# Kernel optimization log

Measured on AMD Instinct MI355X. Metric: run time of the kernel, lower is better.

## Reference

```python
import jax, jax.numpy as jnp
import numpy as np

SEQ, B, IN, H, L = 256, 512, 300, 512, 256
EPS = 1e-5


def setup_inputs() -> dict:
    key = jax.random.key(0)
    ks = jax.random.split(key, 10)
    s_ih = 1.0 / np.sqrt(H)
    return {
        "x": jax.random.normal(ks[0], (SEQ, B, IN), dtype=jnp.float32),
        "W_ih": jax.random.normal(ks[1], (4 * H, IN), dtype=jnp.float32) * s_ih,
        "W_hh": jax.random.normal(ks[2], (4 * H, H), dtype=jnp.float32) * s_ih,
        "b_ih": jax.random.normal(ks[3], (4 * H,), dtype=jnp.float32) * s_ih,
        "b_hh": jax.random.normal(ks[4], (4 * H,), dtype=jnp.float32) * s_ih,
        "bn1_gamma": jnp.ones((H,), dtype=jnp.float32),
        "bn1_beta": jnp.zeros((H,), dtype=jnp.float32),
        "W1": jax.random.normal(ks[5], (L, H), dtype=jnp.float32) / np.sqrt(H),
        "b1": jax.random.normal(ks[6], (L,), dtype=jnp.float32) * 0.01,
        "bn2_gamma": jnp.ones((L,), dtype=jnp.float32),
        "bn2_beta": jnp.zeros((L,), dtype=jnp.float32),
        "W2": jax.random.normal(ks[7], (1, L), dtype=jnp.float32) / np.sqrt(L),
        "b2": jax.random.normal(ks[8], (1,), dtype=jnp.float32) * 0.01,
    }


def _batchnorm(x, gamma, beta):
    # training-mode BatchNorm1d: batch statistics, biased variance
    mean = jnp.mean(x, axis=0)
    var = jnp.var(x, axis=0)
    return (x - mean) * jax.lax.rsqrt(var + EPS) * gamma + beta


def reference(x, W_ih, W_hh, b_ih, b_hh, bn1_gamma, bn1_beta, W1, b1,
              bn2_gamma, bn2_beta, W2, b2):
    # Pre-compute the input projection for all timesteps in one big GEMM:
    # [S, B, IN] @ [IN, 4H] -> [S, B, 4H]
    x_proj = jnp.einsum('sbi,gi->sbg', x, W_ih) + b_ih + b_hh

    def step(carry, xt):
        h, c = carry
        gates = xt + h @ W_hh.T  # [B, 4H]
        i, f, g, o = jnp.split(gates, 4, axis=-1)
        i = jax.nn.sigmoid(i)
        f = jax.nn.sigmoid(f)
        g = jnp.tanh(g)
        o = jax.nn.sigmoid(o)
        c = f * c + i * g
        h = o * jnp.tanh(c)
        return (h, c), None

    h0 = jnp.zeros((x.shape[1], H), dtype=x.dtype)
    c0 = jnp.zeros((x.shape[1], H), dtype=x.dtype)
    (h, _c), _ = jax.lax.scan(step, (h0, c0), x_proj)
    # dropout with training=False -> identity

    h = _batchnorm(h, bn1_gamma, bn1_beta)
    h = h @ W1.T + b1
    h = _batchnorm(h, bn2_gamma, bn2_beta)
    h = jax.nn.relu(h)
    out = h @ W2.T + b2            # [B, 1]
    out = 4.0 * jax.nn.sigmoid(out)
    return out.squeeze(-1)         # [B]
```

## Files before the change

### kernel.cpp

```cpp
#include <hip/hip_runtime.h>
#include <math.h>

constexpr int SEQ   = 256;
constexpr int BATCH = 512;
constexpr int INDIM = 300;
constexpr int KIH   = 320;
constexpr int HDIM  = 512;
constexpr int LDIM  = 256;
constexpr int G4    = 4 * HDIM;

typedef _Float16 f16x8 __attribute__((ext_vector_type(8)));
typedef _Float16 f16x4 __attribute__((ext_vector_type(4)));
typedef float    f32x4 __attribute__((ext_vector_type(4)));


__global__ __launch_bounds__(256) void prep_weights_kernel(
    const float* __restrict__ Wih, const float* __restrict__ Whh,
    const float* __restrict__ bih, const float* __restrict__ bhh,
    _Float16* __restrict__ slab, float* __restrict__ bsum)
{
    const int by = blockIdx.x >> 6;
    const int rl = blockIdx.x & 63;
    const int g  = rl >> 4, r = rl & 15;
    const int grow = g * HDIM + by * 16 + r;
    const int tid = threadIdx.x;
    if (tid < 208) {
        const int col0 = tid * 4;
        f16x4 v;
        #pragma unroll
        for (int e = 0; e < 4; ++e) {
            const int col = col0 + e;
            float f;
            if (col < KIH) f = (col < INDIM) ? Wih[(size_t)grow * INDIM + col] : 0.f;
            else           f = Whh[(size_t)grow * HDIM + (col - KIH)];
            v[e] = (_Float16)f;
        }
        *(f16x4*)(slab + ((size_t)(by * 64 + rl)) * 832 + col0) = v;
    } else if (tid == 208) {
        bsum[grow] = bih[grow] + bhh[grow];
    }
}

__global__ __launch_bounds__(256) void prep_x_kernel(
    const float* __restrict__ x, _Float16* __restrict__ xall)
{
    const int rowl = threadIdx.x >> 6;
    const int s    = threadIdx.x & 63;
    const int row  = blockIdx.x * 4 + rowl;
    if (s >= 40) return;
    const int k0 = s * 8;
    const float* xr = x + (size_t)row * INDIM;
    f16x8 v;
    #pragma unroll
    for (int e = 0; e < 8; ++e)
        v[e] = (k0 + e < INDIM) ? (_Float16)xr[k0 + e] : (_Float16)0.f;
    *(f16x8*)(xall + (size_t)row * KIH + k0) = v;
}

__global__ __launch_bounds__(512, 2) void lstm_persist10(
    const _Float16* __restrict__ xall,
    const _Float16* __restrict__ slab,
    _Float16* __restrict__ hb,
    float* __restrict__ h32,
    const float* __restrict__ bsum,
    int* __restrict__ cnt)
{
    __shared__ _Float16 act[13][64][64];
    __shared__ float    Gb2[2][64][68];

    const int tid  = threadIdx.x;
    const int wid  = tid >> 6;
    const int lane = tid & 63;
    const int gg   = wid >> 2;
    const int bh   = (wid >> 1) & 1;
    const int ks   = wid & 1;
    const int l15  = lane & 15;
    const int q4   = lane >> 4;
    const int bx   = blockIdx.x & 7;
    const int by   = blockIdx.x >> 3;
    const int b0   = bx * 64;
    const int hc0  = by * 16;

    f16x8 ws[13][2];
    {
        const _Float16* sb = slab + (size_t)by * 64 * 832
                                  + (size_t)(gg * 32 + l15) * 832 + ks * 32 + q4 * 8;
        #pragma unroll
        for (int ch = 0; ch < 13; ++ch)
            #pragma unroll
            for (int mt = 0; mt < 2; ++mt) {
                const unsigned long long* p = (const unsigned long long*)
                    (sb + (size_t)mt * 16 * 832 + ch * 64);
                union { unsigned long long u[2]; f16x8 v; } w;
                w.u[0] = __hip_atomic_load(p,     __ATOMIC_RELAXED,
                                           __HIP_MEMORY_SCOPE_AGENT);
                w.u[1] = __hip_atomic_load(p + 1, __ATOMIC_RELAXED,
                                           __HIP_MEMORY_SCOPE_AGENT);
                ws[ch][mt] = w.v;
            }
    }

    const int srow  = tid >> 3;
    const int suu   = tid & 7;
    const int wbyte = srow * 128 + ((suu ^ (srow & 7)) << 4);

    int rbyte[2];
    #pragma unroll
    for (int bt = 0; bt < 2; ++bt) {
        const int row  = bh * 32 + bt * 16 + l15;
        const int unit = ks * 4 + q4;
        rbyte[bt] = row * 128 + ((unit ^ (row & 7)) << 4);
    }

    const int bl  = tid >> 3;
    const int j0l = (tid & 7) * 2;
    const int bg  = b0 + bl;
    const int jg  = hc0 + j0l;
    float bsv[4][2];
    #pragma unroll
    for (int g = 0; g < 4; ++g) {
        bsv[g][0] = bsum[g * HDIM + jg];
        bsv[g][1] = bsum[g * HDIM + jg + 1];
    }
    float cv0 = 0.f, cv1 = 0.f;

#define BARX() do { asm volatile("" ::: "memory");                           \
                    __builtin_amdgcn_s_barrier();                            \
                    asm volatile("" ::: "memory"); } while (0)
#define LGKM0() asm volatile("s_waitcnt lgkmcnt(0)" ::: "memory")
#define VM0()   asm volatile("s_waitcnt vmcnt(0)" ::: "memory")

    const _Float16* xpt = xall + (size_t)(b0 + srow) * KIH + suu * 8;
    const _Float16* hpt = hb + (size_t)(b0 + srow) * HDIM + suu * 8;

    f16x8 xcur[5], xnxt[5];
    #pragma unroll
    for (int ch = 0; ch < 5; ++ch)
        xcur[ch] = *(const f16x8*)(xpt + ch * 64);

    for (int t = 0; t < SEQ; ++t) {
        #pragma unroll
        for (int ch = 0; ch < 5; ++ch)
            *(f16x8*)((char*)&act[ch][0][0] + wbyte) = xcur[ch];

        if (t > 0) {
            const int* fp = cnt + bx * 32 + (lane & 31);
            int wd = 0;
            for (;;) {
                const int f = __hip_atomic_load(fp, __ATOMIC_RELAXED,
                                                __HIP_MEMORY_SCOPE_AGENT);
                if (__all(f >= t)) break;
                if (++wd > (1 << 20)) break;
                __builtin_amdgcn_s_sleep(1);
            }
            asm volatile("" ::: "memory");
        }

        {
            const _Float16* hbase = hpt + (size_t)(t & 1) * BATCH * HDIM;
            f16x8 hr[8];
            #pragma unroll
            for (int j = 0; j < 8; ++j) {
                const unsigned long long* p = (const unsigned long long*)
                    (hbase + j * 64);
                union { unsigned long long u[2]; f16x8 v; } hv;
                hv.u[0] = __hip_atomic_load(p,     __ATOMIC_RELAXED,
                                            __HIP_MEMORY_SCOPE_AGENT);
                hv.u[1] = __hip_atomic_load(p + 1, __ATOMIC_RELAXED,
                                            __HIP_MEMORY_SCOPE_AGENT);
                hr[j] = hv.v;
            }
            #pragma unroll
            for (int j = 0; j < 8; ++j)
                *(f16x8*)((char*)&act[5 + j][0][0] + wbyte) = hr[j];
        }
        LGKM0(); BARX();

        {
            const _Float16* xnb = xpt + (size_t)(t + 1) * BATCH * KIH;
            #pragma unroll
            for (int ch = 0; ch < 5; ++ch)
                xnxt[ch] = *(const f16x8*)(xnb + ch * 64);
        }

        f32x4 acc00 = {0.f,0.f,0.f,0.f}, acc01 = {0.f,0.f,0.f,0.f};
        f32x4 acc10 = {0.f,0.f,0.f,0.f}, acc11 = {0.f,0.f,0.f,0.f};
        #pragma unroll
        for (int ch = 0; ch < 13; ++ch) {
            const char* base = (const char*)&act[ch][0][0];
            const f16x8 bf0 = *(const f16x8*)(base + rbyte[0]);
            const f16x8 bf1 = *(const f16x8*)(base + rbyte[1]);
            acc00 = __builtin_amdgcn_mfma_f32_16x16x32_f16(ws[ch][0], bf0, acc00, 0, 0, 0);
            acc01 = __builtin_amdgcn_mfma_f32_16x16x32_f16(ws[ch][0], bf1, acc01, 0, 0, 0);
            acc10 = __builtin_amdgcn_mfma_f32_16x16x32_f16(ws[ch][1], bf0, acc10, 0, 0, 0);
            acc11 = __builtin_amdgcn_mfma_f32_16x16x32_f16(ws[ch][1], bf1, acc11, 0, 0, 0);
        }

        #pragma unroll
        for (int q = 0; q < 4; ++q) {
            Gb2[ks][gg * 32 +      q4 * 4 + q][bh * 32 +      l15] = acc00[q];
            Gb2[ks][gg * 32 +      q4 * 4 + q][bh * 32 + 16 + l15] = acc01[q];
            Gb2[ks][gg * 32 + 16 + q4 * 4 + q][bh * 32 +      l15] = acc10[q];
            Gb2[ks][gg * 32 + 16 + q4 * 4 + q][bh * 32 + 16 + l15] = acc11[q];
        }
        LGKM0(); BARX();

        {
            float pre[4][2];
            #pragma unroll
            for (int g = 0; g < 4; ++g) {
                pre[g][0] = Gb2[0][g * 16 + j0l    ][bl]
                          + Gb2[1][g * 16 + j0l    ][bl] + bsv[g][0];
                pre[g][1] = Gb2[0][g * 16 + j0l + 1][bl]
                          + Gb2[1][g * 16 + j0l + 1][bl] + bsv[g][1];
            }
            float hv0, hv1;
            {
                float vi = 1.f / (1.f + __expf(-pre[0][0]));
                float vf = 1.f / (1.f + __expf(-pre[1][0]));
                float vg = 1.f - 2.f / (__expf(2.f * pre[2][0]) + 1.f);
                float vo = 1.f / (1.f + __expf(-pre[3][0]));
                const float cc = vf * cv0 + vi * vg;
                cv0 = cc;
                hv0 = vo * (1.f - 2.f / (__expf(2.f * cc) + 1.f));
            }
            {
                float vi = 1.f / (1.f + __expf(-pre[0][1]));
                float vf = 1.f / (1.f + __expf(-pre[1][1]));
                float vg = 1.f - 2.f / (__expf(2.f * pre[2][1]) + 1.f);
                float vo = 1.f / (1.f + __expf(-pre[3][1]));
                const float cc = vf * cv1 + vi * vg;
                cv1 = cc;
                hv1 = vo * (1.f - 2.f / (__expf(2.f * cc) + 1.f));
            }
            union { unsigned int u; _Float16 v[2]; } hu;
            hu.v[0] = (_Float16)hv0; hu.v[1] = (_Float16)hv1;
            _Float16* hbw = hb + (size_t)((t + 1) & 1) * BATCH * HDIM;
            __hip_atomic_store((unsigned int*)(hbw + (size_t)bg * HDIM + jg),
                               hu.u, __ATOMIC_RELAXED, __HIP_MEMORY_SCOPE_AGENT);
            if (t == SEQ - 1) {
                float* hp = h32 + (size_t)bg * HDIM + jg;
                hp[0] = hv0; hp[1] = hv1;
            }
        }
        VM0(); BARX();
        if (tid == 0)
            __hip_atomic_store(&cnt[bx * 32 + by], t + 1, __ATOMIC_RELAXED,
                               __HIP_MEMORY_SCOPE_AGENT);

        #pragma unroll
        for (int ch = 0; ch < 5; ++ch) xcur[ch] = xnxt[ch];
    }
#undef BARX
#undef LGKM0
#undef VM0
}

__global__ __launch_bounds__(256) void prep_kernel(
    const float* __restrict__ Wih, const float* __restrict__ Whh,
    const float* __restrict__ bih, const float* __restrict__ bhh,
    _Float16* __restrict__ Wihc, _Float16* __restrict__ Whhc,
    float* __restrict__ bsum)
{
    const int g = blockIdx.x;
    for (int col = threadIdx.x; col < KIH; col += 256)
        Wihc[(size_t)g * KIH + col] =
            (col < INDIM) ? (_Float16)Wih[(size_t)g * INDIM + col] : (_Float16)0.f;
    for (int col = threadIdx.x; col < HDIM; col += 256)
        Whhc[(size_t)g * HDIM + col] = (_Float16)Whh[(size_t)g * HDIM + col];
    if (threadIdx.x == 0) bsum[g] = bih[g] + bhh[g];
}

__global__ __launch_bounds__(256) void fused_step_kernel(
    const float* __restrict__ xt, const _Float16* __restrict__ Wihc,
    const _Float16* __restrict__ Whhc, const float* __restrict__ bsum,
    float* __restrict__ c, float* __restrict__ h)
{
    __shared__ _Float16 As[32][72];
    __shared__ _Float16 Bs[128][72];
    __shared__ float    Gb[4][32][36];

    const int tid = threadIdx.x;
    const int b0  = blockIdx.x * 32;
    const int hc0 = blockIdx.y * 32;
    const int wid  = tid >> 6;
    const int lane = tid & 63;

    f32x4 acc[2][2] = {};
    const int arow = tid >> 3;
    const int ac8  = (tid & 7) * 8;
    const int brr  = tid >> 1;
    const int bseg = (tid & 1) * 32;

    for (int phase = 0; phase < 2; ++phase) {
        const float* Asrc = phase ? h : xt;
        const _Float16* Bsrc = phase ? Whhc : Wihc;
        const int Kpad = phase ? HDIM : KIH;
        const int Kval = phase ? HDIM : INDIM;
        const int astr = phase ? HDIM : INDIM;

        for (int k0 = 0; k0 < Kpad; k0 += 64) {
            const int gk = k0 + ac8;
            const float* pa = Asrc + (size_t)(b0 + arow) * astr + gk;
            float4 u = {0.f,0.f,0.f,0.f}, v = {0.f,0.f,0.f,0.f};
            if (gk + 3 < Kval)  u = *(const float4*)pa;
            if (gk + 7 < Kval)  v = *(const float4*)(pa + 4);
            f16x8 a8;
            a8[0]=(_Float16)u.x; a8[1]=(_Float16)u.y; a8[2]=(_Float16)u.z; a8[3]=(_Float16)u.w;
            a8[4]=(_Float16)v.x; a8[5]=(_Float16)v.y; a8[6]=(_Float16)v.z; a8[7]=(_Float16)v.w;
            const int grow = (brr >> 5) * HDIM + hc0 + (brr & 31);
            const _Float16* pb = Bsrc + (size_t)grow * Kpad + k0 + bseg;
            f16x8 w0 = *(const f16x8*)(pb + 0);
            f16x8 w1 = *(const f16x8*)(pb + 8);
            f16x8 w2 = *(const f16x8*)(pb + 16);
            f16x8 w3 = *(const f16x8*)(pb + 24);
            __syncthreads();
            *(f16x8*)&As[arow][ac8] = a8;
            *(f16x8*)&Bs[brr][bseg + 0]  = w0;
            *(f16x8*)&Bs[brr][bseg + 8]  = w1;
            *(f16x8*)&Bs[brr][bseg + 16] = w2;
            *(f16x8*)&Bs[brr][bseg + 24] = w3;
            __syncthreads();
            const int lr = lane & 15;
            const int lk = (lane >> 4) * 8;
            #pragma unroll
            for (int kf = 0; kf < 2; ++kf) {
                const int kl = kf * 32 + lk;
                f16x8 a0 = *(const f16x8*)&As[lr][kl];
                f16x8 a1 = *(const f16x8*)&As[16 + lr][kl];
                f16x8 bb0 = *(const f16x8*)&Bs[wid * 32 + lr][kl];
                f16x8 bb1 = *(const f16x8*)&Bs[wid * 32 + 16 + lr][kl];
                acc[0][0] = __builtin_amdgcn_mfma_f32_16x16x32_f16(a0, bb0, acc[0][0], 0, 0, 0);
                acc[0][1] = __builtin_amdgcn_mfma_f32_16x16x32_f16(a0, bb1, acc[0][1], 0, 0, 0);
                acc[1][0] = __builtin_amdgcn_mfma_f32_16x16x32_f16(a1, bb0, acc[1][0], 0, 0, 0);
                acc[1][1] = __builtin_amdgcn_mfma_f32_16x16x32_f16(a1, bb1, acc[1][1], 0, 0, 0);
            }
        }
    }
    __syncthreads();
    {
        const int cn = lane & 15;
        const int rbq = (lane >> 4) * 4;
        #pragma unroll
        for (int mi = 0; mi < 2; ++mi)
            #pragma unroll
            for (int ni = 0; ni < 2; ++ni)
                #pragma unroll
                for (int r = 0; r < 4; ++r)
                    Gb[wid][mi * 16 + rbq + r][ni * 16 + cn] = acc[mi][ni][r];
    }
    __syncthreads();
    {
        const int bl  = tid >> 3;
        const int jl0 = (tid & 7) * 4;
        const int gb  = b0 + bl;
        const int gj  = hc0 + jl0;
        const f32x4 ig = *(const f32x4*)&Gb[0][bl][jl0];
        const f32x4 fg = *(const f32x4*)&Gb[1][bl][jl0];
        const f32x4 gg = *(const f32x4*)&Gb[2][bl][jl0];
        const f32x4 og = *(const f32x4*)&Gb[3][bl][jl0];
        const f32x4 bi = *(const f32x4*)&bsum[0 * HDIM + gj];
        const f32x4 bf = *(const f32x4*)&bsum[1 * HDIM + gj];
        const f32x4 bg = *(const f32x4*)&bsum[2 * HDIM + gj];
        const f32x4 bo = *(const f32x4*)&bsum[3 * HDIM + gj];
        float* cp = c + (size_t)gb * HDIM + gj;
        float* hp = h + (size_t)gb * HDIM + gj;
        f32x4 cvv = *(const f32x4*)cp;
        f32x4 hv;
        #pragma unroll
        for (int q = 0; q < 4; ++q) {
            const float iv = 1.f / (1.f + __expf(-(ig[q] + bi[q])));
            const float fv = 1.f / (1.f + __expf(-(fg[q] + bf[q])));
            const float gv = tanhf(gg[q] + bg[q]);
            const float ov = 1.f / (1.f + __expf(-(og[q] + bo[q])));
            const float cc = fv * cvv[q] + iv * gv;
            cvv[q] = cc;
            hv[q] = ov * tanhf(cc);
        }
        *(f32x4*)cp = cvv;
        *(f32x4*)hp = hv;
    }
}

__global__ __launch_bounds__(256) void bn_stats_kernel(
    const float* __restrict__ X, int nfeat,
    const float* __restrict__ gamma, const float* __restrict__ beta,
    float* __restrict__ s, float* __restrict__ t)
{
    const int f = blockIdx.x * 256 + threadIdx.x;
    if (f >= nfeat) return;
    float sum = 0.f, sq = 0.f;
    for (int b = 0; b < BATCH; ++b) {
        const float v = X[(size_t)b * nfeat + f];
        sum += v; sq += v * v;
    }
    const float mean = sum * (1.f / BATCH);
    const float var  = sq * (1.f / BATCH) - mean * mean;
    const float rstd = rsqrtf(var + 1e-5f);
    const float sc   = gamma[f] * rstd;
    s[f] = sc;
    t[f] = beta[f] - mean * sc;
}

__global__ __launch_bounds__(256) void fc1_kernel(
    const float* __restrict__ h, const float* __restrict__ s1,
    const float* __restrict__ t1, const float* __restrict__ W1,
    const float* __restrict__ b1, float* __restrict__ out1)
{
    const int b = blockIdx.x;
    const int l = threadIdx.x;
    const float* hbp = h  + (size_t)b * HDIM;
    const float* wl  = W1 + (size_t)l * HDIM;
    float acc = 0.f;
    for (int k = 0; k < HDIM; ++k)
        acc += (hbp[k] * s1[k] + t1[k]) * wl[k];
    out1[(size_t)b * LDIM + l] = acc + b1[l];
}

__global__ __launch_bounds__(256) void final_kernel(
    const float* __restrict__ out1, const float* __restrict__ s2,
    const float* __restrict__ t2, const float* __restrict__ W2,
    const float* __restrict__ b2, float* __restrict__ out)
{
    const int b = blockIdx.x;
    float v = out1[(size_t)b * LDIM + threadIdx.x];
    v = v * s2[threadIdx.x] + t2[threadIdx.x];
    v = fmaxf(v, 0.f);
    v *= W2[threadIdx.x];
    #pragma unroll
    for (int off = 32; off > 0; off >>= 1) v += __shfl_down(v, off);
    __shared__ float red[4];
    if ((threadIdx.x & 63) == 0) red[threadIdx.x >> 6] = v;
    __syncthreads();
    if (threadIdx.x == 0) {
        const float ssum = red[0] + red[1] + red[2] + red[3] + b2[0];
        out[b] = 4.f / (1.f + expf(-ssum));
    }
}

extern "C" void kernel_launch(void* const* d_in, const int* in_sizes, int n_in,
                              void* d_out, int out_size, void* d_ws, size_t ws_size,
                              hipStream_t stream) {
    const float* x   = (const float*)d_in[0];
    const float* Wih = (const float*)d_in[1];
    const float* Whh = (const float*)d_in[2];
    const float* bih = (const float*)d_in[3];
    const float* bhh = (const float*)d_in[4];
    const float* g1  = (const float*)d_in[5];
    const float* be1 = (const float*)d_in[6];
    const float* W1  = (const float*)d_in[7];
    const float* b1  = (const float*)d_in[8];
    const float* g2  = (const float*)d_in[9];
    const float* be2 = (const float*)d_in[10];
    const float* W2  = (const float*)d_in[11];
    const float* b2  = (const float*)d_in[12];
    float* out = (float*)d_out;

    const size_t SZ_XALL = (size_t)(SEQ + 1) * BATCH * KIH * 2;
    const size_t SZ_SLAB = (size_t)32 * 64 * 832 * 2;
    const size_t SZ_HB   = (size_t)2 * BATCH * HDIM * 2;
    const size_t SZ_H32  = (size_t)BATCH * HDIM * 4;
    const size_t SZ_BSUM = (size_t)G4 * 4;
    const size_t SZ_CNT  = (size_t)SEQ * 8 * 4;
    const size_t SZ_ST   = (size_t)(HDIM * 2 + LDIM * 2) * 4;
    const size_t SZ_OUT1 = (size_t)BATCH * LDIM * 4;
    const size_t NEED = SZ_XALL + SZ_SLAB + SZ_HB + SZ_H32 + SZ_BSUM +
                        SZ_CNT + SZ_ST + SZ_OUT1;

    if (ws_size >= NEED) {
        char* p = (char*)d_ws;
        _Float16* xall = (_Float16*)p;           p += SZ_XALL;
        _Float16* slab = (_Float16*)p;           p += SZ_SLAB;
        _Float16* hbuf = (_Float16*)p;           p += SZ_HB;
        float* h32     = (float*)p;              p += SZ_H32;
        float* bsum    = (float*)p;              p += SZ_BSUM;
        int*   cnt     = (int*)p;                p += SZ_CNT;
        float* s1 = (float*)p;                   p += HDIM * 4;
        float* t1 = (float*)p;                   p += HDIM * 4;
        float* s2 = (float*)p;                   p += LDIM * 4;
        float* t2 = (float*)p;                   p += LDIM * 4;
        float* out1 = (float*)p;

        hipMemsetAsync(hbuf, 0, SZ_HB, stream);
        hipMemsetAsync(cnt, 0, SZ_CNT, stream);
        prep_weights_kernel<<<2048, 256, 0, stream>>>(Wih, Whh, bih, bhh, slab, bsum);
        prep_x_kernel<<<SEQ * 128, 256, 0, stream>>>(x, xall);

        lstm_persist10<<<dim3(256), dim3(512), 0, stream>>>(
            xall, slab, hbuf, h32, bsum, cnt);

        bn_stats_kernel<<<2, 256, 0, stream>>>(h32, HDIM, g1, be1, s1, t1);
        fc1_kernel<<<BATCH, 256, 0, stream>>>(h32, s1, t1, W1, b1, out1);
        bn_stats_kernel<<<1, 256, 0, stream>>>(out1, LDIM, g2, be2, s2, t2);
        final_kernel<<<BATCH, 256, 0, stream>>>(out1, s2, t2, W2, b2, out);
    } else {
        float* ws   = (float*)d_ws;
        float* h    = ws;
        float* c    = h + BATCH * HDIM;
        float* bsum = c + BATCH * HDIM;
        float* s1   = bsum + G4;
        float* t1   = s1 + HDIM;
        float* s2   = t1 + HDIM;
        float* t2   = s2 + LDIM;
        float* out1 = t2 + LDIM;
        _Float16* Wihc = (_Float16*)(out1 + (size_t)BATCH * LDIM);
        _Float16* Whhc = Wihc + (size_t)G4 * KIH;

        hipMemsetAsync(h, 0, (size_t)2 * BATCH * HDIM * sizeof(float), stream);
        prep_kernel<<<G4, 256, 0, stream>>>(Wih, Whh, bih, bhh, Wihc, Whhc, bsum);
        const dim3 sgrid(BATCH / 32, HDIM / 32);
        for (int t = 0; t < SEQ; ++t) {
            fused_step_kernel<<<sgrid, 256, 0, stream>>>(
                x + (size_t)t * BATCH * INDIM, Wihc, Whhc, bsum, c, h);
        }
        bn_stats_kernel<<<2, 256, 0, stream>>>(h, HDIM, g1, be1, s1, t1);
        fc1_kernel<<<BATCH, 256, 0, stream>>>(h, s1, t1, W1, b1, out1);
        bn_stats_kernel<<<1, 256, 0, stream>>>(out1, LDIM, g2, be2, s2, t2);
        final_kernel<<<BATCH, 256, 0, stream>>>(out1, s2, t2, W2, b2, out);
    }
}
```

Baseline: 1.419 ms.

## Overlap input-projection MFMAs with cross-block flag wait in persistent LSTM

Splits the per-step gate GEMM into the x-projection chunks and the recurrent h chunks. Waves 1-7 compute the five x chunks while wave 0 spins on the inter-block completion counters, and wave 0 does its own x chunks after the barrier. Only the h-dependent chunks then wait for the new hidden state. This hides part of the global synchronisation latency behind independent MFMA work, at the cost of an extra barrier per step and a less even spread of work across waves.

```diff
diff --git a/kernel.cpp b/kernel.cpp
--- a/kernel.cpp
+++ b/kernel.cpp
@@ -57,7 +57,7 @@
     *(f16x8*)(xall + (size_t)row * KIH + k0) = v;
 }
 
-__global__ __launch_bounds__(512, 2) void lstm_persist10(
+__global__ __launch_bounds__(512, 2) void lstm_persist11(
     const _Float16* __restrict__ xall,
     const _Float16* __restrict__ slab,
     _Float16* __restrict__ hb,
@@ -130,6 +130,16 @@
 #define LGKM0() asm volatile("s_waitcnt lgkmcnt(0)" ::: "memory")
 #define VM0()   asm volatile("s_waitcnt vmcnt(0)" ::: "memory")
 
+#define MFMA_CHUNK(CH) do {                                                  \
+        const char* base = (const char*)&act[CH][0][0];                      \
+        const f16x8 bf0 = *(const f16x8*)(base + rbyte[0]);                  \
+        const f16x8 bf1 = *(const f16x8*)(base + rbyte[1]);                  \
+        acc00 = __builtin_amdgcn_mfma_f32_16x16x32_f16(ws[CH][0], bf0, acc00, 0, 0, 0); \
+        acc01 = __builtin_amdgcn_mfma_f32_16x16x32_f16(ws[CH][0], bf1, acc01, 0, 0, 0); \
+        acc10 = __builtin_amdgcn_mfma_f32_16x16x32_f16(ws[CH][1], bf0, acc10, 0, 0, 0); \
+        acc11 = __builtin_amdgcn_mfma_f32_16x16x32_f16(ws[CH][1], bf1, acc11, 0, 0, 0); \
+    } while (0)
+
     const _Float16* xpt = xall + (size_t)(b0 + srow) * KIH + suu * 8;
     const _Float16* hpt = hb + (size_t)(b0 + srow) * HDIM + suu * 8;
 
@@ -142,23 +152,33 @@
         #pragma unroll
         for (int ch = 0; ch < 5; ++ch)
             *(f16x8*)((char*)&act[ch][0][0] + wbyte) = xcur[ch];
-
-        if (t > 0) {
-            const int* fp = cnt + bx * 32 + (lane & 31);
-            int wd = 0;
-            for (;;) {
-                const int f = __hip_atomic_load(fp, __ATOMIC_RELAXED,
-                                                __HIP_MEMORY_SCOPE_AGENT);
-                if (__all(f >= t)) break;
-                if (++wd > (1 << 20)) break;
-                __builtin_amdgcn_s_sleep(1);
-            }
-            asm volatile("" ::: "memory");
-        }
-
+        LGKM0(); BARX();
+
+        f32x4 acc00 = {0.f,0.f,0.f,0.f}, acc01 = {0.f,0.f,0.f,0.f};
+        f32x4 acc10 = {0.f,0.f,0.f,0.f}, acc11 = {0.f,0.f,0.f,0.f};
+
+        if (wid == 0) {
+            if (t > 0) {
+                const int* fp = cnt + bx * 32 + (lane & 31);
+                int wd = 0;
+                for (;;) {
+                    const int f = __hip_atomic_load(fp, __ATOMIC_RELAXED,
+                                                    __HIP_MEMORY_SCOPE_AGENT);
+                    if (__all(f >= t)) break;
+                    if (++wd > (1 << 20)) break;
+                    __builtin_amdgcn_s_sleep(2);
+                }
+                asm volatile("" ::: "memory");
+            }
+        } else {
+            MFMA_CHUNK(0); MFMA_CHUNK(1); MFMA_CHUNK(2);
+            MFMA_CHUNK(3); MFMA_CHUNK(4);
+        }
+        BARX();
+
+        f16x8 hr[8];
         {
             const _Float16* hbase = hpt + (size_t)(t & 1) * BATCH * HDIM;
-            f16x8 hr[8];
             #pragma unroll
             for (int j = 0; j < 8; ++j) {
                 const unsigned long long* p = (const unsigned long long*)
@@ -170,31 +190,24 @@
                                             __HIP_MEMORY_SCOPE_AGENT);
                 hr[j] = hv.v;
             }
-            #pragma unroll
-            for (int j = 0; j < 8; ++j)
-                *(f16x8*)((char*)&act[5 + j][0][0] + wbyte) = hr[j];
-        }
-        LGKM0(); BARX();
-
+        }
+        if (wid == 0) {
+            MFMA_CHUNK(0); MFMA_CHUNK(1); MFMA_CHUNK(2);
+            MFMA_CHUNK(3); MFMA_CHUNK(4);
+        }
         {
             const _Float16* xnb = xpt + (size_t)(t + 1) * BATCH * KIH;
             #pragma unroll
             for (int ch = 0; ch < 5; ++ch)
                 xnxt[ch] = *(const f16x8*)(xnb + ch * 64);
         }
-
-        f32x4 acc00 = {0.f,0.f,0.f,0.f}, acc01 = {0.f,0.f,0.f,0.f};
-        f32x4 acc10 = {0.f,0.f,0.f,0.f}, acc11 = {0.f,0.f,0.f,0.f};
-        #pragma unroll
-        for (int ch = 0; ch < 13; ++ch) {
-            const char* base = (const char*)&act[ch][0][0];
-            const f16x8 bf0 = *(const f16x8*)(base + rbyte[0]);
-            const f16x8 bf1 = *(const f16x8*)(base + rbyte[1]);
-            acc00 = __builtin_amdgcn_mfma_f32_16x16x32_f16(ws[ch][0], bf0, acc00, 0, 0, 0);
-            acc01 = __builtin_amdgcn_mfma_f32_16x16x32_f16(ws[ch][0], bf1, acc01, 0, 0, 0);
-            acc10 = __builtin_amdgcn_mfma_f32_16x16x32_f16(ws[ch][1], bf0, acc10, 0, 0, 0);
-            acc11 = __builtin_amdgcn_mfma_f32_16x16x32_f16(ws[ch][1], bf1, acc11, 0, 0, 0);
-        }
+        #pragma unroll
+        for (int j = 0; j < 8; ++j)
+            *(f16x8*)((char*)&act[5 + j][0][0] + wbyte) = hr[j];
+        LGKM0(); BARX();
+
+        MFMA_CHUNK(5); MFMA_CHUNK(6); MFMA_CHUNK(7); MFMA_CHUNK(8);
+        MFMA_CHUNK(9); MFMA_CHUNK(10); MFMA_CHUNK(11); MFMA_CHUNK(12);
 
         #pragma unroll
         for (int q = 0; q < 4; ++q) {
@@ -254,6 +267,7 @@
 #undef BARX
 #undef LGKM0
 #undef VM0
+#undef MFMA_CHUNK
 }
 
 __global__ __launch_bounds__(256) void prep_kernel(
@@ -486,7 +500,7 @@
         prep_weights_kernel<<<2048, 256, 0, stream>>>(Wih, Whh, bih, bhh, slab, bsum);
         prep_x_kernel<<<SEQ * 128, 256, 0, stream>>>(x, xall);
 
-        lstm_persist10<<<dim3(256), dim3(512), 0, stream>>>(
+        lstm_persist11<<<dim3(256), dim3(512), 0, stream>>>(
             xall, slab, hbuf, h32, bsum, cnt);
 
         bn_stats_kernel<<<2, 256, 0, stream>>>(h32, HDIM, g1, be1, s1, t1);
```

Result: faster. 1.281 ms, median of 2 (-9.7%).
